# Optimization experiments

Measured on AMD Instinct MI355X. Metric: run time of the kernel, lower is better.

## Reference

```python
import jax, jax.numpy as jnp
import numpy as np

T, B, C, H = 512, 1024, 128, 256

def setup_inputs() -> dict:
    key = jax.random.key(0)
    ks = jax.random.split(key, 7)
    s = 1.0 / np.sqrt(H)
    return {
        "in_sequences": jax.random.normal(ks[0], (T, B, C), dtype=jnp.float32),
        "start_hidden": jnp.zeros((2, 1, B, H), dtype=jnp.float32),
        "W_ih": jax.random.normal(ks[1], (4 * H, C), dtype=jnp.float32) * s,
        "W_hh": jax.random.normal(ks[2], (4 * H, H), dtype=jnp.float32) * s,
        "b_ih": jax.random.normal(ks[3], (4 * H,), dtype=jnp.float32) * s,
        "b_hh": jax.random.normal(ks[4], (4 * H,), dtype=jnp.float32) * s,
        "sequence_breaks": jax.random.randint(ks[5], (T, B), 0, 2) > 0,
    }

def reference(in_sequences, start_hidden, W_ih, W_hh, b_ih, b_hh, sequence_breaks):
    # Single-layer LSTM over time with hidden-state reset at sequence breaks.
    # Gate order follows torch: i, f, g, o.
    b = b_ih + b_hh  # [4H]

    def step(carry, inp):
        h, c = carry                      # [B, H] each
        x, brk = inp                      # x: [B, C], brk: [B] bool
        gates = x @ W_ih.T + h @ W_hh.T + b   # [B, 4H]
        i, f, g, o = jnp.split(gates, 4, axis=-1)
        c_new = jax.nn.sigmoid(f) * c + jax.nn.sigmoid(i) * jnp.tanh(g)
        h_new = jax.nn.sigmoid(o) * jnp.tanh(c_new)
        # reset state AFTER emitting output, for the next timestep
        keep = (~brk)[:, None].astype(h_new.dtype)
        return (h_new * keep, c_new * keep), h_new

    h0 = start_hidden[0, 0]  # [B, H]
    c0 = start_hidden[1, 0]
    _, outs = jax.lax.scan(step, (h0, c0), (in_sequences, sequence_breaks))
    return outs  # [T, B, H]
```

## Files before the change

### kernel.cpp

```cpp
#include <hip/hip_runtime.h>


typedef __attribute__((ext_vector_type(8))) short bf16x8_t;
typedef __attribute__((ext_vector_type(4))) float f32x4_t;

#define RFIX 16

__device__ __forceinline__ unsigned short f2b(float f) {
  unsigned u = __float_as_uint(f);
  unsigned r = (u + 0x7FFFu + ((u >> 16) & 1u)) >> 16;
  return (unsigned short)r;
}

__device__ __forceinline__ bf16x8_t pack8(float4 a, float4 b) {
  bf16x8_t v;
  v[0] = (short)f2b(a.x); v[1] = (short)f2b(a.y);
  v[2] = (short)f2b(a.z); v[3] = (short)f2b(a.w);
  v[4] = (short)f2b(b.x); v[5] = (short)f2b(b.y);
  v[6] = (short)f2b(b.z); v[7] = (short)f2b(b.w);
  return v;
}

__device__ __forceinline__ float sigm(float v) { return 1.f / (1.f + __expf(-v)); }
__device__ __forceinline__ float tanh_f(float v) { return 1.f - 2.f / (__expf(2.f * v) + 1.f); }


__global__ void k_rmap(const int* __restrict__ brk, unsigned short* __restrict__ rmap,
                       unsigned short* __restrict__ wgcnt) {
  __shared__ unsigned lh[512];
  for (int i = threadIdx.x; i < 512; i += 256) lh[i] = 0;
  __syncthreads();
  int idx = blockIdx.x * 256 + threadIdx.x;
  int t = idx >> 10, b = idx & 1023;
  int r = 0, tt = t - 1;
  while (tt >= 0 && brk[tt * 1024 + b] == 0) { ++r; --tt; }
  rmap[idx] = (unsigned short)r;
  atomicAdd(&lh[r], 1u);
  __syncthreads();
  for (int i = threadIdx.x; i < 512; i += 256)
    wgcnt[i * 2048 + blockIdx.x] = (unsigned short)lh[i];
}

__global__ void k_scanwg(const unsigned short* __restrict__ wgcnt,
                         unsigned* __restrict__ wgbase, unsigned* __restrict__ hist) {
  int r = blockIdx.x;
  int i = threadIdx.x;
  const unsigned short* src = wgcnt + r * 2048;
  unsigned* dst = wgbase + r * 2048;
  unsigned short lv[8];
  unsigned s = 0;
#pragma unroll
  for (int j = 0; j < 8; ++j) { lv[j] = src[i * 8 + j]; s += lv[j]; }
  __shared__ unsigned ts[256];
  ts[i] = s;
  __syncthreads();
  for (int d = 1; d < 256; d <<= 1) {
    unsigned t = (i >= d) ? ts[i - d] : 0u;
    __syncthreads();
    ts[i] += t;
    __syncthreads();
  }
  unsigned run = ts[i] - s;
#pragma unroll
  for (int j = 0; j < 8; ++j) { dst[i * 8 + j] = run; run += lv[j]; }
  if (i == 255) hist[r] = ts[255];
}

__global__ void k_scan(const unsigned* __restrict__ hist, unsigned* __restrict__ offs) {
  __shared__ unsigned h[512];
  int i = threadIdx.x;
  h[i] = hist[i];
  __syncthreads();
  unsigned s = 0;
  for (int j = 0; j < i; ++j) s += h[j];
  offs[i] = s;
}

__global__ void k_scatter(const unsigned short* __restrict__ rmap,
                          const unsigned* __restrict__ wgbase,
                          const unsigned* __restrict__ offs,
                          unsigned* __restrict__ list, unsigned* __restrict__ slotmap) {
  __shared__ unsigned lh[512];
  for (int i = threadIdx.x; i < 512; i += 256) lh[i] = 0;
  __syncthreads();
  int idx = blockIdx.x * 256 + threadIdx.x;
  int rr = rmap[idx];
  unsigned lpos = atomicAdd(&lh[rr], 1u);
  unsigned loc = wgbase[rr * 2048 + blockIdx.x] + lpos;
  list[offs[rr] + loc] = (unsigned)idx;
  slotmap[idx] = loc;
}

__global__ void k_xprep(const float* __restrict__ x, unsigned short* __restrict__ xbf) {
  size_t i = ((size_t)blockIdx.x * 256 + threadIdx.x) * 16;
  float4 a0 = *(const float4*)(x + i);
  float4 a1 = *(const float4*)(x + i + 4);
  float4 a2 = *(const float4*)(x + i + 8);
  float4 a3 = *(const float4*)(x + i + 12);
  *(bf16x8_t*)(xbf + i) = pack8(a0, a1);
  *(bf16x8_t*)(xbf + i + 8) = pack8(a2, a3);
}


__global__ void k_wprep(const float* __restrict__ Wih, const float* __restrict__ Whh,
                        unsigned short* __restrict__ Wb2) {
  int id = blockIdx.x * 256 + threadIdx.x;
  int lane = id & 63;
  int kc = (id >> 6) % 12;
  int b2 = id / (64 * 12);
  int n = lane & 15, l4 = lane >> 4;
  int g = n >> 2, hc = n & 3;
  int hcol = b2 * 4 + hc;
  int gr = g * 256 + hcol;
  int k0 = kc * 32 + l4 * 8;
  const float* s = (k0 < 128) ? (Wih + (size_t)gr * 128 + k0)
                              : (Whh + (size_t)gr * 256 + (k0 - 128));
  float4 v0 = *(const float4*)s;
  float4 v1 = *(const float4*)(s + 4);
  *(bf16x8_t*)(Wb2 + (size_t)id * 8) = pack8(v0, v1);
}


template<bool HASH, bool SEQ>
__global__ __launch_bounds__(256, 4)
void k_step(const float* __restrict__ x, const unsigned short* __restrict__ xbf,
            float* __restrict__ out, unsigned short* __restrict__ hbf,
            const int* __restrict__ brk, const unsigned short* __restrict__ Wb2,
            const float* __restrict__ bih, const float* __restrict__ bhh,
            const unsigned* __restrict__ list, const unsigned* __restrict__ hist,
            const unsigned* __restrict__ offs, const unsigned* __restrict__ slotmap,
            float* __restrict__ cst, int rstep, int G)
{
  constexpr int NC = HASH ? 6 : 2;
  __shared__ __align__(16) unsigned short Ab[2][64][64];
  __shared__ __align__(16) float Gx[4][256];
  __shared__ unsigned lidx[64];
  __shared__ unsigned lslot[64];

  unsigned n, base;
  if (SEQ) { n = 1024; base = 0; }
  else     { n = hist[rstep]; base = offs[rstep]; }
  if (n == 0) return;

  const int jb = blockIdx.x / G;
  const int gq = blockIdx.x % G;
  const unsigned ntiles = (n + 63u) >> 6;
  const unsigned cr = (ntiles + (unsigned)G - 1u) / (unsigned)G;
  unsigned t_lo = (unsigned)gq * cr;
  if (t_lo >= ntiles) return;
  unsigned t_hi = t_lo + cr; if (t_hi > ntiles) t_hi = ntiles;

  const int tid = threadIdx.x;
  const int lane = tid & 63;
  const int cq = tid >> 6;
  const int l15 = lane & 15, l4 = lane >> 4;
  const int g = l15 >> 2, hc = l15 & 3;

  const unsigned short* wp0 =
      Wb2 + ((size_t)((jb * 4 + cq) * 12) * 64 + lane) * 8;

  const int hcol = jb * 16 + cq * 4 + hc;
  const float bias = bih[g * 256 + hcol] + bhh[g * 256 + hcol];

  const int srow = tid >> 2, kq = tid & 3;

  for (unsigned tile = t_lo; tile < t_hi; ++tile) {
    const unsigned mbase = tile << 6;
    unsigned sgi = mbase + (unsigned)srow;
    bool svalid = sgi < n;
    int st = 0, sb = 0;
    if (svalid) {
      if (SEQ) { st = rstep; sb = (int)sgi; }
      else { unsigned v = list[base + sgi]; st = (int)(v >> 10); sb = (int)(v & 1023); }
    }
    const size_t rowid = (size_t)(st * 1024 + sb);
    bool hok = false;
    if (HASH && svalid) hok = !SEQ || (brk[(st - 1) * 1024 + sb] == 0);

    if (kq == 0) lidx[srow] = (unsigned)((st << 10) | sb);
    unsigned slotv = 0x80000000u;
    if (!SEQ && svalid && kq == 0) {
      int bv = (st + 1 < 512) ? brk[(size_t)st * 1024 + sb] : 1;
      if (HASH) {
        unsigned s0 = slotmap[(unsigned)((st - (rstep - 1)) * 1024 + sb)];
        slotv = s0 | (bv == 0 ? 0u : 0x80000000u);
      } else {
        slotv = (bv == 0) ? slotmap[(unsigned)((st + 1) * 1024 + sb)] : 0x80000000u;
      }
    }

    const unsigned short* wp = wp0;
    asm volatile("" : "+v"(wp));

    auto loadA = [&](int cc, bf16x8_t& v0, bf16x8_t& v1) {
      v0 = (bf16x8_t)0; v1 = (bf16x8_t)0;
      if (!svalid) return;
      int ks = cc * 64 + kq * 16;
      if (!HASH || cc < 2) {
        if (xbf) {
          const unsigned short* s = xbf + rowid * 128 + ks;
          v0 = *(const bf16x8_t*)s; v1 = *(const bf16x8_t*)(s + 8);
        } else {
          const float* s = x + rowid * 128 + ks;
          float4 a0 = *(const float4*)s,       a1 = *(const float4*)(s + 4);
          float4 a2 = *(const float4*)(s + 8), a3 = *(const float4*)(s + 12);
          v0 = pack8(a0, a1); v1 = pack8(a2, a3);
        }
      } else {
        if (!hok) return;
        int kh = ks - 128;
        if (!SEQ && hbf) {
          const unsigned short* s = hbf + rowid * 256 + kh;
          v0 = *(const bf16x8_t*)s; v1 = *(const bf16x8_t*)(s + 8);
        } else {
          const float* s = out + (rowid - 1024) * 256 + kh;
          float4 a0 = *(const float4*)s,       a1 = *(const float4*)(s + 4);
          float4 a2 = *(const float4*)(s + 8), a3 = *(const float4*)(s + 12);
          v0 = pack8(a0, a1); v1 = pack8(a2, a3);
        }
      }
    };
    auto storeA = [&](int buf, bf16x8_t v0, bf16x8_t v1) {
      int s0 = (kq * 2) ^ (srow & 7);
      int s1 = (kq * 2 + 1) ^ (srow & 7);
      *(bf16x8_t*)(&Ab[buf][srow][s0 * 8]) = v0;
      *(bf16x8_t*)(&Ab[buf][srow][s1 * 8]) = v1;
    };

    f32x4_t acc[4];
#pragma unroll
    for (int rf = 0; rf < 4; ++rf)
      acc[rf] = (f32x4_t){0.f, 0.f, 0.f, 0.f};

    bf16x8_t wa = *(const bf16x8_t*)(wp);
    bf16x8_t wb = *(const bf16x8_t*)(wp + 512);
    {
      bf16x8_t p0, p1;
      loadA(0, p0, p1);
      storeA(0, p0, p1);
    }
    __syncthreads();

#pragma unroll
    for (int c = 0; c < NC; ++c) {
      bf16x8_t nwa, nwb, n0, n1;
      if (c + 1 < NC) {
        nwa = *(const bf16x8_t*)(wp + (size_t)(2 * (c + 1)) * 512);
        nwb = *(const bf16x8_t*)(wp + (size_t)(2 * (c + 1) + 1) * 512);
        loadA(c + 1, n0, n1);
      }
#pragma unroll
      for (int kf = 0; kf < 2; ++kf) {
        bf16x8_t av[4];
#pragma unroll
        for (int rf = 0; rf < 4; ++rf) {
          int row = rf * 16 + l15;
          int slot = (kf * 4 + l4) ^ (row & 7);
          av[rf] = *(const bf16x8_t*)(&Ab[c & 1][row][slot * 8]);
        }
        if (kf == 0) {
#pragma unroll
          for (int rf = 0; rf < 4; ++rf)
            acc[rf] = __builtin_amdgcn_mfma_f32_16x16x32_bf16(av[rf], wa, acc[rf], 0, 0, 0);
        } else {
#pragma unroll
          for (int rf = 0; rf < 4; ++rf)
            acc[rf] = __builtin_amdgcn_mfma_f32_16x16x32_bf16(av[rf], wb, acc[rf], 0, 0, 0);
        }
      }
      if (c + 1 < NC) {
        storeA((c + 1) & 1, n0, n1);
        wa = nwa; wb = nwb;
      }
      if (c == NC - 1 && !SEQ && kq == 0) lslot[srow] = slotv;
      __syncthreads();
    }

    float* gw = &Gx[cq][0];
#pragma unroll
    for (int rf = 0; rf < 4; ++rf) {
#pragma unroll
      for (int reg = 0; reg < 4; ++reg) {
        int row_l = l4 * 4 + reg;
        float raw = acc[rf][reg] + bias;
        float v = (g == 2) ? tanh_f(raw) : sigm(raw);
        int cell = row_l * 4 + (hc ^ (row_l & 3));
        gw[cell * 4 + g] = v;
      }
      {
        int row_l = lane >> 2, hc4 = lane & 3;
        int cell = row_l * 4 + (hc4 ^ (row_l & 3));
        f32x4_t gv = *(const f32x4_t*)(gw + cell * 4);
        unsigned gi = mbase + (unsigned)(rf * 16 + row_l);
        if (gi < n) {
          int t, bb;
          unsigned sl = 0x80000000u;
          if (SEQ) { t = rstep; bb = (int)gi; }
          else {
            unsigned lv = lidx[rf * 16 + row_l];
            t = (int)(lv >> 10); bb = (int)(lv & 1023);
            sl = lslot[rf * 16 + row_l];
          }
          int oc = jb * 16 + cq * 4 + hc4;
          float cprev = 0.f;
          if (HASH) {
            if (SEQ) {
              cprev = (brk[(t - 1) * 1024 + bb] != 0) ? 0.f : cst[(size_t)bb * 256 + oc];
            } else {
              cprev = cst[(size_t)(sl & 0x7FFFFFFFu) * 256 + oc];
            }
          }
          float cn = gv[1] * cprev + gv[0] * gv[2];
          float hn = gv[3] * tanh_f(cn);
          out[((size_t)(t * 1024 + bb)) * 256 + oc] = hn;
          if (SEQ) {
            cst[(size_t)bb * 256 + oc] = cn;
          } else if (!(sl >> 31)) {
            cst[(size_t)(sl & 0x7FFFFFFFu) * 256 + oc] = cn;
            if (hbf) hbf[((size_t)((t + 1) * 1024 + bb)) * 256 + oc] = f2b(hn);
          }
        }
      }
    }
    __syncthreads();
  }
}

__global__ void k_cleanup(const float* __restrict__ x, float* __restrict__ out,
                          const int* __restrict__ brk,
                          const float* __restrict__ Wih, const float* __restrict__ Whh,
                          const float* __restrict__ bih, const float* __restrict__ bhh,
                          const unsigned* __restrict__ list, const unsigned* __restrict__ hist,
                          const unsigned* __restrict__ offs, const unsigned* __restrict__ slotmap,
                          float* __restrict__ cst)
{
  const int j = threadIdx.x;
  for (int r = RFIX + 1; r < 512; ++r) {
    unsigned n = hist[r];
    if (n == 0) continue;
    for (unsigned i = 0; i < n; ++i) {
      unsigned v = list[offs[r] + i];
      int t = (int)(v >> 10), bb = (int)(v & 1023);
      unsigned slot = slotmap[(unsigned)((t - (r - 1)) * 1024 + bb)];
      const float* xr = x + (size_t)(t * 1024 + bb) * 128;
      const float* hr = out + (size_t)((t - 1) * 1024 + bb) * 256;
      float a0 = bih[j] + bhh[j];
      float a1 = bih[j + 256] + bhh[j + 256];
      float a2 = bih[j + 512] + bhh[j + 512];
      float a3 = bih[j + 768] + bhh[j + 768];
      for (int k = 0; k < 128; ++k) {
        float xv = xr[k];
        a0 += xv * Wih[(size_t)j * 128 + k];
        a1 += xv * Wih[(size_t)(j + 256) * 128 + k];
        a2 += xv * Wih[(size_t)(j + 512) * 128 + k];
        a3 += xv * Wih[(size_t)(j + 768) * 128 + k];
      }
      for (int k = 0; k < 256; ++k) {
        float hv = hr[k];
        a0 += hv * Whh[(size_t)j * 256 + k];
        a1 += hv * Whh[(size_t)(j + 256) * 256 + k];
        a2 += hv * Whh[(size_t)(j + 512) * 256 + k];
        a3 += hv * Whh[(size_t)(j + 768) * 256 + k];
      }
      float cprev = cst[(size_t)slot * 256 + j];
      float ig = sigm(a0), fg = sigm(a1), gg = tanh_f(a2), og = sigm(a3);
      float cn = fg * cprev + ig * gg;
      float hn = og * tanh_f(cn);
      out[(size_t)(t * 1024 + bb) * 256 + j] = hn;
      if (t + 1 < 512 && brk[t * 1024 + bb] == 0) cst[(size_t)slot * 256 + j] = cn;
      __threadfence();
      __syncthreads();
    }
  }
}


extern "C" void kernel_launch(void* const* d_in, const int* in_sizes, int n_in,
                              void* d_out, int out_size, void* d_ws, size_t ws_size,
                              hipStream_t stream) {
  (void)in_sizes; (void)n_in; (void)out_size;
  const float* x   = (const float*)d_in[0];
  const float* Wih = (const float*)d_in[2];
  const float* Whh = (const float*)d_in[3];
  const float* bih = (const float*)d_in[4];
  const float* bhh = (const float*)d_in[5];
  const int*   brk = (const int*)d_in[6];
  float* out = (float*)d_out;

  const size_t MB = 1024 * 1024;
  char* ws = (char*)d_ws;
  unsigned* slotmap    = (unsigned*)(ws);
  unsigned short* wgcnt= (unsigned short*)(ws);
  unsigned* list       = (unsigned*)(ws + 2 * MB);
  unsigned* hist       = (unsigned*)(ws + 4 * MB);
  unsigned* offs       = (unsigned*)(ws + 4 * MB + 4096);
  unsigned short* rmap = (unsigned short*)(ws + 4 * MB + 64 * 1024);
  unsigned short* Wb2  = (unsigned short*)(ws + 4 * MB + 64 * 1024);
  unsigned* wgbase     = (unsigned*)(ws + 5 * MB + 64 * 1024);
  const size_t off_cst = 10 * MB;
  const size_t off_xbf = off_cst + (size_t)262144 * 256 * 4;
  const size_t off_hbf = off_xbf + (size_t)512 * 1024 * 128 * 2;
  float* cst           = (float*)(ws + off_cst);
  unsigned short* xbf  = (unsigned short*)(ws + off_xbf);
  unsigned short* hbf  = (unsigned short*)(ws + off_hbf);

  const size_t need_base = off_xbf;
  const size_t need_xbf  = off_hbf;
  const size_t need_hbf  = off_hbf + (size_t)512 * 1024 * 256 * 2;

  if (ws_size >= need_base) {
    const unsigned short* xbf_p = (ws_size >= need_xbf) ? xbf : nullptr;
    unsigned short* hbf_p = (ws_size >= need_hbf) ? hbf : nullptr;
    k_rmap<<<dim3(2048), dim3(256), 0, stream>>>(brk, rmap, wgcnt);
    k_scanwg<<<dim3(512), dim3(256), 0, stream>>>(wgcnt, wgbase, hist);
    k_scan<<<dim3(1), dim3(512), 0, stream>>>(hist, offs);
    k_scatter<<<dim3(2048), dim3(256), 0, stream>>>(rmap, wgbase, offs, list, slotmap);
    k_wprep<<<dim3(192), dim3(256), 0, stream>>>(Wih, Whh, Wb2);
    if (xbf_p) k_xprep<<<dim3(16384), dim3(256), 0, stream>>>(x, xbf);
    k_step<false, false><<<dim3(16 * 128), dim3(256), 0, stream>>>(
        x, xbf_p, out, hbf_p, brk, Wb2, bih, bhh, list, hist, offs, slotmap, cst, 0, 128);
    for (int r = 1; r <= RFIX; ++r) {
      int G = 4096 >> (r + 1);
      if (G > 128) G = 128;
      if (G < 16) G = 16;
      k_step<true, false><<<dim3(16 * G), dim3(256), 0, stream>>>(
          x, xbf_p, out, hbf_p, brk, Wb2, bih, bhh, list, hist, offs, slotmap, cst, r, G);
    }
    k_cleanup<<<dim3(1), dim3(256), 0, stream>>>(
        x, out, brk, Wih, Whh, bih, bhh, list, hist, offs, slotmap, cst);
  } else {
    float* cfb = (float*)ws;
    unsigned short* wfb = (unsigned short*)(ws + 2 * MB);
    k_wprep<<<dim3(192), dim3(256), 0, stream>>>(Wih, Whh, wfb);
    k_step<false, true><<<dim3(16 * 16), dim3(256), 0, stream>>>(
        x, nullptr, out, nullptr, brk, wfb, bih, bhh, nullptr, nullptr, nullptr, nullptr, cfb, 0, 16);
    for (int t = 1; t < 512; ++t) {
      k_step<true, true><<<dim3(16 * 16), dim3(256), 0, stream>>>(
          x, nullptr, out, nullptr, brk, wfb, bih, bhh, nullptr, nullptr, nullptr, nullptr, cfb, t, 16);
    }
  }
}
```

Measured before the change: 1.751 ms.

## Load A tiles via global_load_lds into full-depth LDS buffers, drop double buffering

The fast path now loads every K-chunk of the activation tile (x and bf16 h) straight from global memory into LDS with global_load_lds, using a swizzled layout in dynamic shared memory sized for all chunks. This replaces the register-staged double-buffered loop and its per-chunk barriers with one barrier before the MFMA loop. The gate buffer aliases the A region in the hash kernel, which needs an extra barrier. The fallback sequential path becomes a separate kernel, and the fast path now requires the full workspace including hbf.

```diff
diff --git a/kernel.cpp b/kernel.cpp
--- a/kernel.cpp
+++ b/kernel.cpp
@@ -23,6 +23,12 @@
 
 __device__ __forceinline__ float sigm(float v) { return 1.f / (1.f + __expf(-v)); }
 __device__ __forceinline__ float tanh_f(float v) { return 1.f - 2.f / (__expf(2.f * v) + 1.f); }
+
+__device__ __forceinline__ void gld16(const void* g, void* l) {
+  __builtin_amdgcn_global_load_lds(
+      (const __attribute__((address_space(1))) void*)g,
+      (__attribute__((address_space(3))) void*)l, 16, 0, 0);
+}
 
 
 __global__ void k_rmap(const int* __restrict__ brk, unsigned short* __restrict__ rmap,
@@ -100,7 +106,6 @@
   *(bf16x8_t*)(xbf + i) = pack8(a0, a1);
   *(bf16x8_t*)(xbf + i + 8) = pack8(a2, a3);
 }
-
 
 __global__ void k_wprep(const float* __restrict__ Wih, const float* __restrict__ Whh,
                         unsigned short* __restrict__ Wb2) {
@@ -121,25 +126,24 @@
 }
 
 
-template<bool HASH, bool SEQ>
+template<bool HASH>
 __global__ __launch_bounds__(256, 4)
-void k_step(const float* __restrict__ x, const unsigned short* __restrict__ xbf,
-            float* __restrict__ out, unsigned short* __restrict__ hbf,
-            const int* __restrict__ brk, const unsigned short* __restrict__ Wb2,
-            const float* __restrict__ bih, const float* __restrict__ bhh,
-            const unsigned* __restrict__ list, const unsigned* __restrict__ hist,
-            const unsigned* __restrict__ offs, const unsigned* __restrict__ slotmap,
-            float* __restrict__ cst, int rstep, int G)
+void k_step_gld(const unsigned short* __restrict__ xbf,
+                float* __restrict__ out, unsigned short* __restrict__ hbf,
+                const int* __restrict__ brk, const unsigned short* __restrict__ Wb2,
+                const float* __restrict__ bih, const float* __restrict__ bhh,
+                const unsigned* __restrict__ list, const unsigned* __restrict__ hist,
+                const unsigned* __restrict__ offs, const unsigned* __restrict__ slotmap,
+                float* __restrict__ cst, int rstep, int G)
 {
   constexpr int NC = HASH ? 6 : 2;
-  __shared__ __align__(16) unsigned short Ab[2][64][64];
-  __shared__ __align__(16) float Gx[4][256];
+  extern __shared__ char dyn[];
+  char* AbRaw = dyn;
+  float* GxAll = (float*)(HASH ? dyn : (dyn + NC * 8192));
   __shared__ unsigned lidx[64];
   __shared__ unsigned lslot[64];
 
-  unsigned n, base;
-  if (SEQ) { n = 1024; base = 0; }
-  else     { n = hist[rstep]; base = offs[rstep]; }
+  unsigned n = hist[rstep], base = offs[rstep];
   if (n == 0) return;
 
   const int jb = blockIdx.x / G;
@@ -163,61 +167,181 @@
   const float bias = bih[g * 256 + hcol] + bhh[g * 256 + hcol];
 
   const int srow = tid >> 2, kq = tid & 3;
+  const int swz = (((lane & 7) ^ ((lane >> 3) & 7)) * 16);
 
   for (unsigned tile = t_lo; tile < t_hi; ++tile) {
     const unsigned mbase = tile << 6;
-    unsigned sgi = mbase + (unsigned)srow;
-    bool svalid = sgi < n;
-    int st = 0, sb = 0;
-    if (svalid) {
-      if (SEQ) { st = rstep; sb = (int)sgi; }
-      else { unsigned v = list[base + sgi]; st = (int)(v >> 10); sb = (int)(v & 1023); }
-    }
-    const size_t rowid = (size_t)(st * 1024 + sb);
-    bool hok = false;
-    if (HASH && svalid) hok = !SEQ || (brk[(st - 1) * 1024 + sb] == 0);
-
-    if (kq == 0) lidx[srow] = (unsigned)((st << 10) | sb);
-    unsigned slotv = 0x80000000u;
-    if (!SEQ && svalid && kq == 0) {
-      int bv = (st + 1 < 512) ? brk[(size_t)st * 1024 + sb] : 1;
-      if (HASH) {
-        unsigned s0 = slotmap[(unsigned)((st - (rstep - 1)) * 1024 + sb)];
-        slotv = s0 | (bv == 0 ? 0u : 0x80000000u);
-      } else {
-        slotv = (bv == 0) ? slotmap[(unsigned)((st + 1) * 1024 + sb)] : 0x80000000u;
+
+    unsigned i0 = mbase + (unsigned)(cq * 16 + (lane >> 3));
+    unsigned i1 = i0 + 8;
+    unsigned rid0 = list[base + (i0 < n ? i0 : n - 1)];
+    unsigned rid1 = list[base + (i1 < n ? i1 : n - 1)];
+    const char* xs0 = (const char*)(xbf + (size_t)rid0 * 128) + swz;
+    const char* xs1 = (const char*)(xbf + (size_t)rid1 * 128) + swz;
+    const char* hs0 = (const char*)(hbf + (size_t)rid0 * 256) + swz;
+    const char* hs1 = (const char*)(hbf + (size_t)rid1 * 256) + swz;
+
+#pragma unroll
+    for (int c = 0; c < NC; ++c) {
+      char* ld0 = AbRaw + c * 8192 + (cq * 16) * 128;
+      char* ld1 = ld0 + 8 * 128;
+      const char *g0, *g1;
+      if (!HASH || c < 2) { g0 = xs0 + c * 128;       g1 = xs1 + c * 128; }
+      else                { g0 = hs0 + (c - 2) * 128; g1 = hs1 + (c - 2) * 128; }
+      gld16(g0, ld0);
+      gld16(g1, ld1);
+    }
+
+    {
+      unsigned sgi = mbase + (unsigned)srow;
+      if (kq == 0) {
+        unsigned v = list[base + (sgi < n ? sgi : n - 1)];
+        lidx[srow] = v;
+        unsigned slotv = 0x80000000u;
+        if (sgi < n) {
+          int st = (int)(v >> 10), sb = (int)(v & 1023);
+          int bv = (st + 1 < 512) ? brk[(size_t)st * 1024 + sb] : 1;
+          if (HASH) {
+            unsigned s0 = slotmap[(unsigned)((st - (rstep - 1)) * 1024 + sb)];
+            slotv = s0 | (bv == 0 ? 0u : 0x80000000u);
+          } else {
+            slotv = (bv == 0) ? slotmap[(unsigned)((st + 1) * 1024 + sb)] : 0x80000000u;
+          }
+        }
+        lslot[srow] = slotv;
       }
     }
 
     const unsigned short* wp = wp0;
     asm volatile("" : "+v"(wp));
+    bf16x8_t wa = *(const bf16x8_t*)(wp);
+    bf16x8_t wb = *(const bf16x8_t*)(wp + 512);
+
+    __syncthreads();
+
+    f32x4_t acc[4];
+#pragma unroll
+    for (int rf = 0; rf < 4; ++rf)
+      acc[rf] = (f32x4_t){0.f, 0.f, 0.f, 0.f};
+
+#pragma unroll
+    for (int c = 0; c < NC; ++c) {
+      bf16x8_t nwa, nwb;
+      if (c + 1 < NC) {
+        nwa = *(const bf16x8_t*)(wp + (size_t)(2 * (c + 1)) * 512);
+        nwb = *(const bf16x8_t*)(wp + (size_t)(2 * (c + 1) + 1) * 512);
+      }
+#pragma unroll
+      for (int kf = 0; kf < 2; ++kf) {
+        bf16x8_t av[4];
+#pragma unroll
+        for (int rf = 0; rf < 4; ++rf) {
+          int row = rf * 16 + l15;
+          int slot = (kf * 4 + l4) ^ (row & 7);
+          av[rf] = *(const bf16x8_t*)(AbRaw + c * 8192 + row * 128 + slot * 16);
+        }
+        if (kf == 0) {
+#pragma unroll
+          for (int rf = 0; rf < 4; ++rf)
+            acc[rf] = __builtin_amdgcn_mfma_f32_16x16x32_bf16(av[rf], wa, acc[rf], 0, 0, 0);
+        } else {
+#pragma unroll
+          for (int rf = 0; rf < 4; ++rf)
+            acc[rf] = __builtin_amdgcn_mfma_f32_16x16x32_bf16(av[rf], wb, acc[rf], 0, 0, 0);
+        }
+      }
+      if (c + 1 < NC) { wa = nwa; wb = nwb; }
+    }
+
+    if (HASH) __syncthreads();
+
+    float* gw = GxAll + cq * 256;
+#pragma unroll
+    for (int rf = 0; rf < 4; ++rf) {
+#pragma unroll
+      for (int reg = 0; reg < 4; ++reg) {
+        int row_l = l4 * 4 + reg;
+        float raw = acc[rf][reg] + bias;
+        float v = (g == 2) ? tanh_f(raw) : sigm(raw);
+        int cell = row_l * 4 + (hc ^ (row_l & 3));
+        gw[cell * 4 + g] = v;
+      }
+      {
+        int row_l = lane >> 2, hc4 = lane & 3;
+        int cell = row_l * 4 + (hc4 ^ (row_l & 3));
+        f32x4_t gv = *(const f32x4_t*)(gw + cell * 4);
+        unsigned gi = mbase + (unsigned)(rf * 16 + row_l);
+        if (gi < n) {
+          unsigned lv = lidx[rf * 16 + row_l];
+          int t = (int)(lv >> 10), bb = (int)(lv & 1023);
+          unsigned sl = lslot[rf * 16 + row_l];
+          int oc = jb * 16 + cq * 4 + hc4;
+          float cprev = 0.f;
+          if (HASH) cprev = cst[(size_t)(sl & 0x7FFFFFFFu) * 256 + oc];
+          float cn = gv[1] * cprev + gv[0] * gv[2];
+          float hn = gv[3] * tanh_f(cn);
+          out[((size_t)(t * 1024 + bb)) * 256 + oc] = hn;
+          if (!(sl >> 31)) {
+            cst[(size_t)(sl & 0x7FFFFFFFu) * 256 + oc] = cn;
+            hbf[((size_t)((t + 1) * 1024 + bb)) * 256 + oc] = f2b(hn);
+          }
+        }
+      }
+    }
+    __syncthreads();
+  }
+}
+
+template<bool HASH>
+__global__ __launch_bounds__(256, 4)
+void k_step_seq(const float* __restrict__ x, float* __restrict__ out,
+                const int* __restrict__ brk, const unsigned short* __restrict__ Wb2,
+                const float* __restrict__ bih, const float* __restrict__ bhh,
+                float* __restrict__ cst, int rstep, int G)
+{
+  constexpr int NC = HASH ? 6 : 2;
+  __shared__ __align__(16) unsigned short Ab[2][64][64];
+  __shared__ __align__(16) float Gx[4][256];
+
+  const int jb = blockIdx.x / G;
+  const int gq = blockIdx.x % G;
+  const unsigned n = 1024;
+  const unsigned ntiles = 16;
+  const unsigned cr = (ntiles + (unsigned)G - 1u) / (unsigned)G;
+  unsigned t_lo = (unsigned)gq * cr;
+  if (t_lo >= ntiles) return;
+  unsigned t_hi = t_lo + cr; if (t_hi > ntiles) t_hi = ntiles;
+
+  const int tid = threadIdx.x;
+  const int lane = tid & 63;
+  const int cq = tid >> 6;
+  const int l15 = lane & 15, l4 = lane >> 4;
+  const int g = l15 >> 2, hc = l15 & 3;
+  const unsigned short* wp0 = Wb2 + ((size_t)((jb * 4 + cq) * 12) * 64 + lane) * 8;
+  const int hcol = jb * 16 + cq * 4 + hc;
+  const float bias = bih[g * 256 + hcol] + bhh[g * 256 + hcol];
+  const int srow = tid >> 2, kq = tid & 3;
+
+  for (unsigned tile = t_lo; tile < t_hi; ++tile) {
+    const unsigned mbase = tile << 6;
+    int st = rstep, sb = (int)(mbase + (unsigned)srow);
+    const size_t rowid = (size_t)(st * 1024 + sb);
+    bool hok = HASH && (brk[(st - 1) * 1024 + sb] == 0);
 
     auto loadA = [&](int cc, bf16x8_t& v0, bf16x8_t& v1) {
       v0 = (bf16x8_t)0; v1 = (bf16x8_t)0;
-      if (!svalid) return;
       int ks = cc * 64 + kq * 16;
       if (!HASH || cc < 2) {
-        if (xbf) {
-          const unsigned short* s = xbf + rowid * 128 + ks;
-          v0 = *(const bf16x8_t*)s; v1 = *(const bf16x8_t*)(s + 8);
-        } else {
-          const float* s = x + rowid * 128 + ks;
-          float4 a0 = *(const float4*)s,       a1 = *(const float4*)(s + 4);
-          float4 a2 = *(const float4*)(s + 8), a3 = *(const float4*)(s + 12);
-          v0 = pack8(a0, a1); v1 = pack8(a2, a3);
-        }
+        const float* s = x + rowid * 128 + ks;
+        float4 a0 = *(const float4*)s,       a1 = *(const float4*)(s + 4);
+        float4 a2 = *(const float4*)(s + 8), a3 = *(const float4*)(s + 12);
+        v0 = pack8(a0, a1); v1 = pack8(a2, a3);
       } else {
         if (!hok) return;
-        int kh = ks - 128;
-        if (!SEQ && hbf) {
-          const unsigned short* s = hbf + rowid * 256 + kh;
-          v0 = *(const bf16x8_t*)s; v1 = *(const bf16x8_t*)(s + 8);
-        } else {
-          const float* s = out + (rowid - 1024) * 256 + kh;
-          float4 a0 = *(const float4*)s,       a1 = *(const float4*)(s + 4);
-          float4 a2 = *(const float4*)(s + 8), a3 = *(const float4*)(s + 12);
-          v0 = pack8(a0, a1); v1 = pack8(a2, a3);
-        }
+        const float* s = out + (rowid - 1024) * 256 + (ks - 128);
+        float4 a0 = *(const float4*)s,       a1 = *(const float4*)(s + 4);
+        float4 a2 = *(const float4*)(s + 8), a3 = *(const float4*)(s + 12);
+        v0 = pack8(a0, a1); v1 = pack8(a2, a3);
       }
     };
     auto storeA = [&](int buf, bf16x8_t v0, bf16x8_t v1) {
@@ -229,16 +353,13 @@
 
     f32x4_t acc[4];
 #pragma unroll
-    for (int rf = 0; rf < 4; ++rf)
-      acc[rf] = (f32x4_t){0.f, 0.f, 0.f, 0.f};
-
+    for (int rf = 0; rf < 4; ++rf) acc[rf] = (f32x4_t){0.f, 0.f, 0.f, 0.f};
+
+    const unsigned short* wp = wp0;
+    asm volatile("" : "+v"(wp));
     bf16x8_t wa = *(const bf16x8_t*)(wp);
     bf16x8_t wb = *(const bf16x8_t*)(wp + 512);
-    {
-      bf16x8_t p0, p1;
-      loadA(0, p0, p1);
-      storeA(0, p0, p1);
-    }
+    { bf16x8_t p0, p1; loadA(0, p0, p1); storeA(0, p0, p1); }
     __syncthreads();
 
 #pragma unroll
@@ -268,11 +389,7 @@
             acc[rf] = __builtin_amdgcn_mfma_f32_16x16x32_bf16(av[rf], wb, acc[rf], 0, 0, 0);
         }
       }
-      if (c + 1 < NC) {
-        storeA((c + 1) & 1, n0, n1);
-        wa = nwa; wb = nwb;
-      }
-      if (c == NC - 1 && !SEQ && kq == 0) lslot[srow] = slotv;
+      if (c + 1 < NC) { storeA((c + 1) & 1, n0, n1); wa = nwa; wb = nwb; }
       __syncthreads();
     }
 
@@ -291,35 +408,15 @@
         int row_l = lane >> 2, hc4 = lane & 3;
         int cell = row_l * 4 + (hc4 ^ (row_l & 3));
         f32x4_t gv = *(const f32x4_t*)(gw + cell * 4);
-        unsigned gi = mbase + (unsigned)(rf * 16 + row_l);
-        if (gi < n) {
-          int t, bb;
-          unsigned sl = 0x80000000u;
-          if (SEQ) { t = rstep; bb = (int)gi; }
-          else {
-            unsigned lv = lidx[rf * 16 + row_l];
-            t = (int)(lv >> 10); bb = (int)(lv & 1023);
-            sl = lslot[rf * 16 + row_l];
-          }
-          int oc = jb * 16 + cq * 4 + hc4;
-          float cprev = 0.f;
-          if (HASH) {
-            if (SEQ) {
-              cprev = (brk[(t - 1) * 1024 + bb] != 0) ? 0.f : cst[(size_t)bb * 256 + oc];
-            } else {
-              cprev = cst[(size_t)(sl & 0x7FFFFFFFu) * 256 + oc];
-            }
-          }
-          float cn = gv[1] * cprev + gv[0] * gv[2];
-          float hn = gv[3] * tanh_f(cn);
-          out[((size_t)(t * 1024 + bb)) * 256 + oc] = hn;
-          if (SEQ) {
-            cst[(size_t)bb * 256 + oc] = cn;
-          } else if (!(sl >> 31)) {
-            cst[(size_t)(sl & 0x7FFFFFFFu) * 256 + oc] = cn;
-            if (hbf) hbf[((size_t)((t + 1) * 1024 + bb)) * 256 + oc] = f2b(hn);
-          }
-        }
+        int t = rstep, bb = (int)(mbase + (unsigned)(rf * 16 + row_l));
+        int oc = jb * 16 + cq * 4 + hc4;
+        float cprev = 0.f;
+        if (HASH)
+          cprev = (brk[(t - 1) * 1024 + bb] != 0) ? 0.f : cst[(size_t)bb * 256 + oc];
+        float cn = gv[1] * cprev + gv[0] * gv[2];
+        float hn = gv[3] * tanh_f(cn);
+        out[((size_t)(t * 1024 + bb)) * 256 + oc] = hn;
+        cst[(size_t)bb * 256 + oc] = cn;
       }
     }
     __syncthreads();
@@ -404,27 +501,31 @@
   unsigned short* xbf  = (unsigned short*)(ws + off_xbf);
   unsigned short* hbf  = (unsigned short*)(ws + off_hbf);
 
-  const size_t need_base = off_xbf;
-  const size_t need_xbf  = off_hbf;
-  const size_t need_hbf  = off_hbf + (size_t)512 * 1024 * 256 * 2;
-
-  if (ws_size >= need_base) {
-    const unsigned short* xbf_p = (ws_size >= need_xbf) ? xbf : nullptr;
-    unsigned short* hbf_p = (ws_size >= need_hbf) ? hbf : nullptr;
+  const size_t need_fast = off_hbf + (size_t)512 * 1024 * 256 * 2;
+
+  if (ws_size >= need_fast) {
+    static bool attr_done = false;
+    if (!attr_done) {
+      hipFuncSetAttribute(reinterpret_cast<const void*>(&k_step_gld<true>),
+                          hipFuncAttributeMaxDynamicSharedMemorySize, 65536);
+      hipFuncSetAttribute(reinterpret_cast<const void*>(&k_step_gld<false>),
+                          hipFuncAttributeMaxDynamicSharedMemorySize, 65536);
+      attr_done = true;
+    }
     k_rmap<<<dim3(2048), dim3(256), 0, stream>>>(brk, rmap, wgcnt);
     k_scanwg<<<dim3(512), dim3(256), 0, stream>>>(wgcnt, wgbase, hist);
     k_scan<<<dim3(1), dim3(512), 0, stream>>>(hist, offs);
     k_scatter<<<dim3(2048), dim3(256), 0, stream>>>(rmap, wgbase, offs, list, slotmap);
     k_wprep<<<dim3(192), dim3(256), 0, stream>>>(Wih, Whh, Wb2);
-    if (xbf_p) k_xprep<<<dim3(16384), dim3(256), 0, stream>>>(x, xbf);
-    k_step<false, false><<<dim3(16 * 128), dim3(256), 0, stream>>>(
-        x, xbf_p, out, hbf_p, brk, Wb2, bih, bhh, list, hist, offs, slotmap, cst, 0, 128);
+    k_xprep<<<dim3(16384), dim3(256), 0, stream>>>(x, xbf);
+    k_step_gld<false><<<dim3(16 * 128), dim3(256), 2 * 8192 + 4096, stream>>>(
+        xbf, out, hbf, brk, Wb2, bih, bhh, list, hist, offs, slotmap, cst, 0, 128);
     for (int r = 1; r <= RFIX; ++r) {
       int G = 4096 >> (r + 1);
       if (G > 128) G = 128;
       if (G < 16) G = 16;
-      k_step<true, false><<<dim3(16 * G), dim3(256), 0, stream>>>(
-          x, xbf_p, out, hbf_p, brk, Wb2, bih, bhh, list, hist, offs, slotmap, cst, r, G);
+      k_step_gld<true><<<dim3(16 * G), dim3(256), 6 * 8192, stream>>>(
+          xbf, out, hbf, brk, Wb2, bih, bhh, list, hist, offs, slotmap, cst, r, G);
     }
     k_cleanup<<<dim3(1), dim3(256), 0, stream>>>(
         x, out, brk, Wih, Whh, bih, bhh, list, hist, offs, slotmap, cst);
@@ -432,11 +533,11 @@
     float* cfb = (float*)ws;
     unsigned short* wfb = (unsigned short*)(ws + 2 * MB);
     k_wprep<<<dim3(192), dim3(256), 0, stream>>>(Wih, Whh, wfb);
-    k_step<false, true><<<dim3(16 * 16), dim3(256), 0, stream>>>(
-        x, nullptr, out, nullptr, brk, wfb, bih, bhh, nullptr, nullptr, nullptr, nullptr, cfb, 0, 16);
+    k_step_seq<false><<<dim3(16 * 16), dim3(256), 0, stream>>>(
+        x, out, brk, wfb, bih, bhh, cfb, 0, 16);
     for (int t = 1; t < 512; ++t) {
-      k_step<true, true><<<dim3(16 * 16), dim3(256), 0, stream>>>(
-          x, nullptr, out, nullptr, brk, wfb, bih, bhh, nullptr, nullptr, nullptr, nullptr, cfb, t, 16);
+      k_step_seq<true><<<dim3(16 * 16), dim3(256), 0, stream>>>(
+          x, out, brk, wfb, bih, bhh, cfb, t, 16);
     }
   }
 }
```

Result: slower. 1.864 ms (+6.5%).
